# Performance work log

Measured on AMD Instinct MI355X. Metric: run time of the kernel, lower is better.

Reference implementation:

```python
import jax, jax.numpy as jnp
import numpy as np

EMBED_DIM = 384
NUM_HEADS = 6
HEAD_DIM = EMBED_DIM // NUM_HEADS


def setup_inputs() -> dict:
    key = jax.random.key(0)
    k1, k2, k3, k4 = jax.random.split(key, 4)
    x = jax.random.normal(k1, (16, EMBED_DIM, 32, 32), dtype=jnp.float32)
    s = 1.0 / np.sqrt(EMBED_DIM)
    w_qkv = jax.random.uniform(k2, (3 * EMBED_DIM, EMBED_DIM), jnp.float32, -s, s)
    w_out = jax.random.uniform(k3, (EMBED_DIM, EMBED_DIM), jnp.float32, -s, s)
    b_out = jax.random.uniform(k4, (EMBED_DIM,), jnp.float32, -s, s)
    return {"x": x, "w_qkv": w_qkv, "w_out": w_out, "b_out": b_out}


def reference(x, w_qkv, w_out, b_out):
    N, C, H, W = x.shape
    S = H * W
    # N,C,H,W -> N,S,C tokens
    tokens = x.reshape(N, C, S).transpose(0, 2, 1)
    qkv = tokens @ w_qkv.T                      # [N,S,3C]
    qkv = qkv.reshape(N, S, 3, NUM_HEADS, HEAD_DIM).transpose(2, 0, 3, 1, 4)
    q, k, v = qkv[0], qkv[1], qkv[2]            # each [N,h,S,d]
    scale = HEAD_DIM ** -0.5
    attn = jax.nn.softmax(jnp.einsum('nhsd,nhtd->nhst', q, k) * scale, axis=-1)
    out = jnp.einsum('nhst,nhtd->nhsd', attn, v)  # [N,h,S,d]
    out = out.transpose(0, 2, 1, 3).reshape(N, S, C)
    out = out @ w_out.T + b_out                 # [N,S,C]
    return out.transpose(0, 2, 1).reshape(N, C, H, W)
```

## Files before the change

kernel.cpp:

```cpp
#include <hip/hip_runtime.h>
#include <hip/hip_bf16.h>

#define EMBED 384
#define SEQ   1024
#define NBATCH 16
#define NH    6
#define HD    64

typedef __bf16 bf16;
typedef bf16  bf16x8 __attribute__((ext_vector_type(8)));
typedef bf16  bf16x4 __attribute__((ext_vector_type(4)));
typedef float f32x4  __attribute__((ext_vector_type(4)));

#define MFMA16(a, b, c) __builtin_amdgcn_mfma_f32_16x16x32_bf16((a), (b), (c), 0, 0, 0)

__device__ __forceinline__ void gload_lds16(const void* g, void* l) {
    __builtin_amdgcn_global_load_lds(
        (const __attribute__((address_space(1))) void*)g,
        (__attribute__((address_space(3))) void*)l, 16, 0, 0);
}

__global__ __launch_bounds__(256) void k_cvt(const float* __restrict__ src,
                                             bf16* __restrict__ dst, int n) {
    int i = blockIdx.x * 256 + threadIdx.x;
    if (i < n) dst[i] = (bf16)src[i];
}

__global__ __launch_bounds__(256) void k_transpose(const float* __restrict__ x,
                                                   bf16* __restrict__ tok) {
    __shared__ bf16 tile[64][66];
    int n  = blockIdx.z;
    int s0 = blockIdx.x * 64;
    int c0 = blockIdx.y * 64;
    int tid = threadIdx.x;

    int sl  = tid & 63;
    int cl0 = tid >> 6;
#pragma unroll
    for (int i = 0; i < 16; ++i) {
        int cl = cl0 + i * 4;
        tile[cl][sl] = (bf16)x[((size_t)n * EMBED + (c0 + cl)) * SEQ + s0 + sl];
    }
    __syncthreads();
    int cl  = tid & 63;
    int sl0 = tid >> 6;
#pragma unroll
    for (int i = 0; i < 16; ++i) {
        int s = sl0 + i * 4;
        tok[((size_t)n * SEQ + (s0 + s)) * EMBED + c0 + cl] = tile[cl][s];
    }
}

__global__ __launch_bounds__(256) void k_qkv(const bf16* __restrict__ tok,
                                             const bf16* __restrict__ wqkv,
                                             bf16* __restrict__ qout,
                                             bf16* __restrict__ kout,
                                             bf16* __restrict__ vtout) {
    __shared__ __align__(16) bf16 At[2][128 * 32];
    __shared__ __align__(16) bf16 Bt[2][128 * 32];

    int b    = blockIdx.x;
    int bm   = b & 7;
    int g    = b >> 3;
    int bn   = g % 9;
    int n    = g / 9;
    int wave = threadIdx.x >> 6;
    int lane = threadIdx.x & 63;
    int row16 = lane & 15;
    int quad  = lane >> 4;
    int sw_base = (wave >> 1) * 64;
    int ow_base = (wave & 1) * 64;

    const bf16* Ag = tok  + ((size_t)n * SEQ + bm * 128) * EMBED;
    const bf16* Bg = wqkv + (size_t)bn * 128 * EMBED;

    int srow = lane >> 2;
    int scol = (lane & 3) * 8;
    auto stage = [&](int kk, int bi) {
#pragma unroll
        for (int j = 0; j < 32; j += 16) {
            int R = wave * 32 + j;
            gload_lds16(Ag + (size_t)(R + srow) * EMBED + kk + scol, &At[bi][R * 32]);
            gload_lds16(Bg + (size_t)(R + srow) * EMBED + kk + scol, &Bt[bi][R * 32]);
        }
    };

    stage(0, 0);

    f32x4 acc[4][4] = {};
    for (int step = 0; step < 12; ++step) {
        __syncthreads();
        int cur = step & 1;
        if (step + 1 < 12) stage((step + 1) * 32, cur ^ 1);

        bf16x8 af[4], bfr[4];
#pragma unroll
        for (int mt = 0; mt < 4; ++mt)
            af[mt] = *reinterpret_cast<const bf16x8*>(
                &At[cur][(sw_base + mt * 16 + row16) * 32 + quad * 8]);
#pragma unroll
        for (int nt = 0; nt < 4; ++nt)
            bfr[nt] = *reinterpret_cast<const bf16x8*>(
                &Bt[cur][(ow_base + nt * 16 + row16) * 32 + quad * 8]);
#pragma unroll
        for (int mt = 0; mt < 4; ++mt)
#pragma unroll
            for (int nt = 0; nt < 4; ++nt)
                acc[mt][nt] = MFMA16(af[mt], bfr[nt], acc[mt][nt]);
    }

    int s_base = bm * 128 + sw_base;
    int o_base = bn * 128 + ow_base;
    int part = (bn * 128) / EMBED;
#pragma unroll
    for (int mt = 0; mt < 4; ++mt)
#pragma unroll
        for (int nt = 0; nt < 4; ++nt) {
            int o   = o_base + nt * 16 + row16;
            int rem = o - part * EMBED;
            int h = rem >> 6;
            int d = rem & 63;
            if (part < 2) {
                bf16* dst = (part == 0) ? qout : kout;
#pragma unroll
                for (int r = 0; r < 4; ++r) {
                    int s = s_base + mt * 16 + quad * 4 + r;
                    dst[(((size_t)n * NH + h) * SEQ + s) * HD + d] = (bf16)acc[mt][nt][r];
                }
            } else {
                int s = s_base + mt * 16 + quad * 4;
                bf16x4 pack;
#pragma unroll
                for (int r = 0; r < 4; ++r) pack[r] = (bf16)acc[mt][nt][r];
                *reinterpret_cast<bf16x4*>(
                    &vtout[(((size_t)n * NH + h) * HD + d) * SEQ + s]) = pack;
            }
        }
}

__global__ __launch_bounds__(256) void k_attn(const bf16* __restrict__ q,
                                              const bf16* __restrict__ kmat,
                                              const bf16* __restrict__ vT,
                                              bf16* __restrict__ ao) {
    __shared__ __align__(16) bf16 ktile[2][64 * 64];
    __shared__ __align__(16) bf16 vtile[2][64 * 64];
    __shared__ __align__(16) bf16 pshare[4][16][72];

    int b     = blockIdx.x;
    int lane8 = b & 7;
    int g     = b >> 3;
    int nh    = (g % 12) * 8 + lane8;
    int qt    = g / 12;
    int n = nh / NH, h = nh % NH;

    int wave = threadIdx.x >> 6;
    int lane = threadIdx.x & 63;
    int row16 = lane & 15;
    int quad  = lane >> 4;
    int sw    = row16 & 7;
    int s_row = qt * 64 + wave * 16;

    const bf16* qh = q    + ((size_t)n * NH + h) * SEQ * HD;
    const bf16* kh = kmat + ((size_t)n * NH + h) * SEQ * HD;
    const bf16* vh = vT   + ((size_t)n * NH + h) * HD * SEQ;

    bf16x8 qf0 = *reinterpret_cast<const bf16x8*>(qh + (size_t)(s_row + row16) * HD + quad * 8);
    bf16x8 qf1 = *reinterpret_cast<const bf16x8*>(qh + (size_t)(s_row + row16) * HD + 32 + quad * 8);

    int r0 = wave * 16;
    auto stage = [&](int t0, int bi) {
#pragma unroll
        for (int j = 0; j < 16; j += 8) {
            int R   = r0 + j;
            int row = R + (lane >> 3);
            int ck  = (lane & 7) ^ (row & 7);
            gload_lds16(kh + (size_t)(t0 + row) * HD + ck * 8,
                        &ktile[bi][R * 64]);
            gload_lds16(vh + (size_t)row * SEQ + t0 + ck * 8,
                        &vtile[bi][R * 64]);
        }
    };

    stage(0, 0);

    float lsum[4] = {0.f, 0.f, 0.f, 0.f};
    f32x4 oacc[4] = {};
    const float kScale = 0.180336879f;

    for (int it = 0; it < 16; ++it) {
        __syncthreads();
        int cur = it & 1;
        if (it + 1 < 16) stage((it + 1) * 64, cur ^ 1);

        const bf16* kb = &ktile[cur][0];
        const bf16* vb = &vtile[cur][0];

        f32x4 sacc[4] = {};
#pragma unroll
        for (int nt = 0; nt < 4; ++nt) {
            bf16x8 kf0 = *reinterpret_cast<const bf16x8*>(
                kb + (nt * 16 + row16) * 64 + ((quad ^ sw) * 8));
            bf16x8 kf1 = *reinterpret_cast<const bf16x8*>(
                kb + (nt * 16 + row16) * 64 + (((4 + quad) ^ sw) * 8));
            sacc[nt] = MFMA16(kf0, qf0, sacc[nt]);
            sacc[nt] = MFMA16(kf1, qf1, sacc[nt]);
        }
#pragma unroll
        for (int nt = 0; nt < 4; ++nt) {
            bf16x4 pk;
            float ps = 0.f;
#pragma unroll
            for (int r = 0; r < 4; ++r) {
                float e = __builtin_amdgcn_exp2f(sacc[nt][r] * kScale);
                ps += e;
                pk[r] = (bf16)e;
            }
            lsum[nt] += ps;
            *reinterpret_cast<bf16x4*>(&pshare[wave][row16][nt * 16 + quad * 4]) = pk;
        }
        __builtin_amdgcn_wave_barrier();
        bf16x8 pf0 = *reinterpret_cast<const bf16x8*>(&pshare[wave][row16][quad * 8]);
        bf16x8 pf1 = *reinterpret_cast<const bf16x8*>(&pshare[wave][row16][32 + quad * 8]);
        __builtin_amdgcn_wave_barrier();
#pragma unroll
        for (int dt = 0; dt < 4; ++dt) {
            bf16x8 vf0 = *reinterpret_cast<const bf16x8*>(
                vb + (dt * 16 + row16) * 64 + ((quad ^ sw) * 8));
            bf16x8 vf1 = *reinterpret_cast<const bf16x8*>(
                vb + (dt * 16 + row16) * 64 + (((4 + quad) ^ sw) * 8));
            oacc[dt] = MFMA16(pf0, vf0, oacc[dt]);
            oacc[dt] = MFMA16(pf1, vf1, oacc[dt]);
        }
    }

    float tot = (lsum[0] + lsum[1]) + (lsum[2] + lsum[3]);
    tot += __shfl_xor(tot, 16, 64);
    tot += __shfl_xor(tot, 32, 64);
    float inv = 1.0f / tot;

    float linv[4];
#pragma unroll
    for (int r = 0; r < 4; ++r) linv[r] = __shfl(inv, quad * 4 + r, 64);

#pragma unroll
    for (int dt = 0; dt < 4; ++dt)
#pragma unroll
        for (int r = 0; r < 4; ++r) {
            int s = s_row + quad * 4 + r;
            int d = dt * 16 + row16;
            ao[((size_t)n * SEQ + s) * EMBED + h * HD + d] = (bf16)(oacc[dt][r] * linv[r]);
        }
}

__global__ __launch_bounds__(256) void k_proj(const bf16* __restrict__ ao,
                                              const bf16* __restrict__ wout,
                                              const float* __restrict__ bout,
                                              float* __restrict__ out) {
    int b    = blockIdx.x;
    int bm   = b & 15;
    int g    = b >> 4;
    int bn   = g % 3;
    int n    = g / 3;
    int wave = threadIdx.x >> 6;
    int lane = threadIdx.x & 63;
    int row16 = lane & 15;
    int quad  = lane >> 4;
    int s_base = bm * 64 + (wave >> 1) * 32;
    int o_base = bn * 128 + (wave & 1) * 64;

    const bf16* A = ao + (size_t)n * SEQ * EMBED;

    f32x4 acc[2][4] = {};
    for (int kk = 0; kk < EMBED; kk += 32) {
        bf16x8 af[2], bfr[4];
#pragma unroll
        for (int mt = 0; mt < 2; ++mt)
            af[mt] = *reinterpret_cast<const bf16x8*>(
                A + (size_t)(s_base + mt * 16 + row16) * EMBED + kk + quad * 8);
#pragma unroll
        for (int nt = 0; nt < 4; ++nt)
            bfr[nt] = *reinterpret_cast<const bf16x8*>(
                wout + (size_t)(o_base + nt * 16 + row16) * EMBED + kk + quad * 8);
#pragma unroll
        for (int mt = 0; mt < 2; ++mt)
#pragma unroll
            for (int nt = 0; nt < 4; ++nt)
                acc[mt][nt] = MFMA16(af[mt], bfr[nt], acc[mt][nt]);
    }

#pragma unroll
    for (int nt = 0; nt < 4; ++nt) {
        int o = o_base + nt * 16 + row16;
        float bias = bout[o];
#pragma unroll
        for (int mt = 0; mt < 2; ++mt) {
            int s = s_base + mt * 16 + quad * 4;
            f32x4 pack;
#pragma unroll
            for (int r = 0; r < 4; ++r) pack[r] = acc[mt][nt][r] + bias;
            *reinterpret_cast<f32x4*>(out + ((size_t)n * EMBED + o) * SEQ + s) = pack;
        }
    }
}

extern "C" void kernel_launch(void* const* d_in, const int* in_sizes, int n_in,
                              void* d_out, int out_size, void* d_ws, size_t ws_size,
                              hipStream_t stream) {
    const float *x = nullptr, *wqkv = nullptr, *wout = nullptr, *bout = nullptr;
    for (int i = 0; i < n_in; ++i) {
        switch (in_sizes[i]) {
            case NBATCH * EMBED * SEQ:   x    = (const float*)d_in[i]; break;
            case 3 * EMBED * EMBED:      wqkv = (const float*)d_in[i]; break;
            case EMBED * EMBED:          wout = (const float*)d_in[i]; break;
            case EMBED:                  bout = (const float*)d_in[i]; break;
        }
    }
    float* out = (float*)d_out;

    bf16* ws = (bf16*)d_ws;
    const size_t NE = (size_t)NBATCH * SEQ * EMBED;
    bf16* tok   = ws;
    bf16* q     = ws + NE;
    bf16* k     = ws + 2 * NE;
    bf16* vT    = ws + 3 * NE;
    bf16* ao    = ws + 4 * NE;
    bf16* wqkvb = ws + 5 * NE;
    bf16* woutb = wqkvb + 3 * EMBED * EMBED;

    const int nqkv = 3 * EMBED * EMBED;
    const int nout = EMBED * EMBED;
    k_cvt<<<dim3((nqkv + 255) / 256), 256, 0, stream>>>(wqkv, wqkvb, nqkv);
    k_cvt<<<dim3((nout + 255) / 256), 256, 0, stream>>>(wout, woutb, nout);

    k_transpose<<<dim3(16, 6, 16), 256, 0, stream>>>(x, tok);
    k_qkv<<<dim3(1152), 256, 0, stream>>>(tok, wqkvb, q, k, vT);
    k_attn<<<dim3(1536), 256, 0, stream>>>(q, k, vT, ao);
    k_proj<<<dim3(768), 256, 0, stream>>>(ao, woutb, bout, out);
}
```

Baseline: 189.1 us.

## Merge weight conversions, fold softmax scale into Q, hoist staging addresses

Replaces the two scalar weight-conversion kernels with a single vectorized float4 kernel that handles both weights, removing one launch. The softmax scale (log2e/sqrt(d)) is now applied once when Q is written in the QKV kernel, so the attention kernel's exp2 loop no longer multiplies every score. Staging address arithmetic in the QKV and attention kernels is hoisted out of the loops, and both main loops are fully unrolled. The cost is that Q is rounded to bf16 after scaling, and full unrolling raises register pressure and code size.

```diff
diff --git a/kernel.cpp b/kernel.cpp
--- a/kernel.cpp
+++ b/kernel.cpp
@@ -14,16 +14,32 @@
 
 #define MFMA16(a, b, c) __builtin_amdgcn_mfma_f32_16x16x32_bf16((a), (b), (c), 0, 0, 0)
 
+#define QSCALE 0.18033688011112042f
+
 __device__ __forceinline__ void gload_lds16(const void* g, void* l) {
     __builtin_amdgcn_global_load_lds(
         (const __attribute__((address_space(1))) void*)g,
         (__attribute__((address_space(3))) void*)l, 16, 0, 0);
 }
 
-__global__ __launch_bounds__(256) void k_cvt(const float* __restrict__ src,
-                                             bf16* __restrict__ dst, int n) {
-    int i = blockIdx.x * 256 + threadIdx.x;
-    if (i < n) dst[i] = (bf16)src[i];
+__global__ __launch_bounds__(256) void k_cvt2(const float* __restrict__ a,
+                                              const float* __restrict__ b,
+                                              bf16* __restrict__ da,
+                                              bf16* __restrict__ db,
+                                              int na, int nb) {
+    int i = (blockIdx.x * 256 + threadIdx.x) * 4;
+    if (i < na) {
+        float4 v = *reinterpret_cast<const float4*>(a + i);
+        bf16x4 o = {(bf16)v.x, (bf16)v.y, (bf16)v.z, (bf16)v.w};
+        *reinterpret_cast<bf16x4*>(da + i) = o;
+    } else {
+        int j = i - na;
+        if (j < nb) {
+            float4 v = *reinterpret_cast<const float4*>(b + j);
+            bf16x4 o = {(bf16)v.x, (bf16)v.y, (bf16)v.z, (bf16)v.w};
+            *reinterpret_cast<bf16x4*>(db + j) = o;
+        }
+    }
 }
 
 __global__ __launch_bounds__(256) void k_transpose(const float* __restrict__ x,
@@ -76,18 +92,22 @@
 
     int srow = lane >> 2;
     int scol = (lane & 3) * 8;
+    const bf16* Abase = Ag + (size_t)(wave * 32 + srow) * EMBED + scol;
+    const bf16* Bbase = Bg + (size_t)(wave * 32 + srow) * EMBED + scol;
+    bf16* AtW = &At[0][0] + wave * 32 * 32;
+    bf16* BtW = &Bt[0][0] + wave * 32 * 32;
+
     auto stage = [&](int kk, int bi) {
-#pragma unroll
-        for (int j = 0; j < 32; j += 16) {
-            int R = wave * 32 + j;
-            gload_lds16(Ag + (size_t)(R + srow) * EMBED + kk + scol, &At[bi][R * 32]);
-            gload_lds16(Bg + (size_t)(R + srow) * EMBED + kk + scol, &Bt[bi][R * 32]);
-        }
+        gload_lds16(Abase + kk,               AtW + bi * 128 * 32);
+        gload_lds16(Abase + kk + 16 * EMBED,  AtW + bi * 128 * 32 + 16 * 32);
+        gload_lds16(Bbase + kk,               BtW + bi * 128 * 32);
+        gload_lds16(Bbase + kk + 16 * EMBED,  BtW + bi * 128 * 32 + 16 * 32);
     };
 
     stage(0, 0);
 
     f32x4 acc[4][4] = {};
+#pragma unroll
     for (int step = 0; step < 12; ++step) {
         __syncthreads();
         int cur = step & 1;
@@ -120,12 +140,18 @@
             int rem = o - part * EMBED;
             int h = rem >> 6;
             int d = rem & 63;
-            if (part < 2) {
-                bf16* dst = (part == 0) ? qout : kout;
+            if (part == 0) {
 #pragma unroll
                 for (int r = 0; r < 4; ++r) {
                     int s = s_base + mt * 16 + quad * 4 + r;
-                    dst[(((size_t)n * NH + h) * SEQ + s) * HD + d] = (bf16)acc[mt][nt][r];
+                    qout[(((size_t)n * NH + h) * SEQ + s) * HD + d] =
+                        (bf16)(acc[mt][nt][r] * QSCALE);
+                }
+            } else if (part == 1) {
+#pragma unroll
+                for (int r = 0; r < 4; ++r) {
+                    int s = s_base + mt * 16 + quad * 4 + r;
+                    kout[(((size_t)n * NH + h) * SEQ + s) * HD + d] = (bf16)acc[mt][nt][r];
                 }
             } else {
                 int s = s_base + mt * 16 + quad * 4;
@@ -167,26 +193,28 @@
     bf16x8 qf0 = *reinterpret_cast<const bf16x8*>(qh + (size_t)(s_row + row16) * HD + quad * 8);
     bf16x8 qf1 = *reinterpret_cast<const bf16x8*>(qh + (size_t)(s_row + row16) * HD + 32 + quad * 8);
 
-    int r0 = wave * 16;
+    int r0   = wave * 16;
+    int srow = r0 + (lane >> 3);
+    int ck   = (lane & 7) ^ (srow & 7);
+    const bf16* kbase = kh + (size_t)srow * HD + ck * 8;
+    const bf16* vbase = vh + (size_t)srow * SEQ + ck * 8;
+    bf16* ktW = &ktile[0][0] + r0 * 64;
+    bf16* vtW = &vtile[0][0] + r0 * 64;
+
     auto stage = [&](int t0, int bi) {
-#pragma unroll
-        for (int j = 0; j < 16; j += 8) {
-            int R   = r0 + j;
-            int row = R + (lane >> 3);
-            int ck  = (lane & 7) ^ (row & 7);
-            gload_lds16(kh + (size_t)(t0 + row) * HD + ck * 8,
-                        &ktile[bi][R * 64]);
-            gload_lds16(vh + (size_t)row * SEQ + t0 + ck * 8,
-                        &vtile[bi][R * 64]);
-        }
+        int lb = bi * 64 * 64;
+        gload_lds16(kbase + (size_t)t0 * HD,           ktW + lb);
+        gload_lds16(kbase + (size_t)t0 * HD + 8 * HD,  ktW + lb + 8 * 64);
+        gload_lds16(vbase + t0,                        vtW + lb);
+        gload_lds16(vbase + t0 + 8 * SEQ,              vtW + lb + 8 * 64);
     };
 
     stage(0, 0);
 
     float lsum[4] = {0.f, 0.f, 0.f, 0.f};
     f32x4 oacc[4] = {};
-    const float kScale = 0.180336879f;
-
+
+#pragma unroll
     for (int it = 0; it < 16; ++it) {
         __syncthreads();
         int cur = it & 1;
@@ -211,7 +239,7 @@
             float ps = 0.f;
 #pragma unroll
             for (int r = 0; r < 4; ++r) {
-                float e = __builtin_amdgcn_exp2f(sacc[nt][r] * kScale);
+                float e = __builtin_amdgcn_exp2f(sacc[nt][r]);
                 ps += e;
                 pk[r] = (bf16)e;
             }
@@ -329,8 +357,8 @@
 
     const int nqkv = 3 * EMBED * EMBED;
     const int nout = EMBED * EMBED;
-    k_cvt<<<dim3((nqkv + 255) / 256), 256, 0, stream>>>(wqkv, wqkvb, nqkv);
-    k_cvt<<<dim3((nout + 255) / 256), 256, 0, stream>>>(wout, woutb, nout);
+    k_cvt2<<<dim3((nqkv + nout) / 4 / 256), 256, 0, stream>>>(wqkv, wout, wqkvb, woutb,
+                                                              nqkv, nout);
 
     k_transpose<<<dim3(16, 6, 16), 256, 0, stream>>>(x, tok);
     k_qkv<<<dim3(1152), 256, 0, stream>>>(tok, wqkvb, q, k, vT);
```

Result: slower. 237.2 us (+25.4%).
